# Kernel tuning notes

Hardware: AMD Instinct MI355X
Metric: run time of the kernel (lower is better)

Reference implementation:

```python
import jax, jax.numpy as jnp
import numpy as np

N_NODES = 100000
N_EDGES = 300000
EMB = 256
L = 5
BN_EPS = 1e-5


def setup_inputs() -> dict:
    key = jax.random.key(0)
    ks = jax.random.split(key, 12)
    x = jax.random.randint(ks[0], (N_NODES, 2), 0, 3, dtype=jnp.int64 if jax.config.jax_enable_x64 else jnp.int32)
    edge_index = jax.random.randint(ks[1], (2, N_EDGES), 0, N_NODES)
    edge_attr = jax.random.randint(ks[2], (N_EDGES, 2), 0, 3)
    s = 0.05
    return {
        "x": x,
        "edge_index": edge_index,
        "edge_attr": edge_attr,
        "x_emb1": jax.random.normal(ks[3], (120, EMB), jnp.float32) * s,
        "x_emb2": jax.random.normal(ks[4], (3, EMB), jnp.float32) * s,
        "edge_e1": jax.random.normal(ks[5], (L, 5, EMB), jnp.float32) * s,
        "edge_e2": jax.random.normal(ks[6], (L, 3, EMB), jnp.float32) * s,
        "W1": jax.random.normal(ks[7], (L, EMB, 2 * EMB), jnp.float32) * s,
        "b1": jnp.zeros((L, 2 * EMB), jnp.float32),
        "W2": jax.random.normal(ks[8], (L, 2 * EMB, EMB), jnp.float32) * s,
        "b2": jnp.zeros((L, EMB), jnp.float32),
        "bn_g": jnp.ones((L, EMB), jnp.float32),
        "bn_b": jnp.zeros((L, EMB), jnp.float32),
    }


def reference(x, edge_index, edge_attr, x_emb1, x_emb2, edge_e1, edge_e2, W1, b1, W2, b2, bn_g, bn_b):
    N = x.shape[0]
    loops = jnp.arange(N, dtype=edge_index.dtype)
    src = jnp.concatenate([edge_index[0], loops])  # [E+N]
    dst = jnp.concatenate([edge_index[1], loops])
    # self-loop edge attr = (4, 0)
    ea0 = jnp.concatenate([edge_attr[:, 0], jnp.full((N,), 4, edge_attr.dtype)])
    ea1 = jnp.concatenate([edge_attr[:, 1], jnp.zeros((N,), edge_attr.dtype)])

    # input atom embedding
    h = x_emb1[x[:, 0]] + x_emb2[x[:, 1]]  # [N, EMB]

    for l in range(L):
        ee = edge_e1[l][ea0] + edge_e2[l][ea1]          # [E+N, EMB]
        msg = h[src] + ee                                # gather + edge message
        agg = jax.ops.segment_sum(msg, dst, num_segments=N)  # scatter-add
        # 2-layer MLP update
        hid = jax.nn.relu(agg @ W1[l] + b1[l])
        h2 = hid @ W2[l] + b2[l]
        # BatchNorm1d (training: batch stats, biased variance)
        mean = jnp.mean(h2, axis=0)
        var = jnp.mean(jnp.square(h2 - mean), axis=0)
        h2 = (h2 - mean) * jax.lax.rsqrt(var + BN_EPS) * bn_g[l] + bn_b[l]
        if l < L - 1:
            h2 = jax.nn.relu(h2)
        h = h2  # drop_ratio = 0 -> dropout is identity
    return h
```

## Files before the change

kernel.cpp:

```cpp
#include <hip/hip_runtime.h>

#define NN 100000
#define NNP 100096
#define NE 300000
#define EMB 256
#define NL 5
#define NPART (NNP / 128)
#define BN_EPS 1e-5f

typedef __attribute__((ext_vector_type(8))) _Float16 half8;
typedef __attribute__((ext_vector_type(4))) float f32x4;

__device__ __forceinline__ ushort f2h(float f) {
  _Float16 h = (_Float16)f;
  return *(ushort*)&h;
}
__device__ __forceinline__ float h2f(ushort u) {
  _Float16 h = *(_Float16*)&u;
  return (float)h;
}

__device__ __forceinline__ void gl2lds16(const ushort* g, ushort* l) {
  __builtin_amdgcn_global_load_lds(
      (const __attribute__((address_space(1))) void*)g,
      (__attribute__((address_space(3))) void*)l, 16, 0, 0);
}

__device__ __forceinline__ ushort* lds_at(ushort* base, int row, int bytecol) {
  return (ushort*)((char*)base + row * 128 + (bytecol ^ ((row & 7) << 4)));
}
__device__ __forceinline__ ushort* lds_ct(ushort* base, int row, int bytecol) {
  return (ushort*)((char*)base + row * 256 + (bytecol ^ ((row & 7) << 4)));
}

__global__ __launch_bounds__(256) void k_embed(ushort* __restrict__ hh,
    const int* __restrict__ x, const float* __restrict__ xe1,
    const float* __restrict__ xe2) {
  const int wid = threadIdx.x >> 6, lane = threadIdx.x & 63;
  const int row = blockIdx.x * 4 + wid;
  const int c = lane << 2;
  const int x0 = x[row * 2], x1 = x[row * 2 + 1];
  float4 a = *(const float4*)(xe1 + (size_t)x0 * EMB + c);
  float4 b = *(const float4*)(xe2 + (size_t)x1 * EMB + c);
  ushort4 o;
  o.x = f2h(a.x + b.x); o.y = f2h(a.y + b.y);
  o.z = f2h(a.z + b.z); o.w = f2h(a.w + b.w);
  *(ushort4*)(hh + (size_t)row * EMB + c) = o;
}

__global__ __launch_bounds__(256) void k_hist(int* __restrict__ deg,
    const int* __restrict__ ei) {
  int e = blockIdx.x * 256 + threadIdx.x;
  if (e < NE) atomicAdd(&deg[ei[NE + e]], 1);
}

__global__ __launch_bounds__(1024) void k_scan(const int* __restrict__ deg,
    int* __restrict__ rowptr, int* __restrict__ cursor) {
  __shared__ int wsum[16], woff[17];
  const int t = threadIdx.x;
  const int lane = t & 63, w = t >> 6;
  int base = 0;
  for (int start = 0; start < NN; start += 1024) {
    const int i = start + t;
    const int v0 = (i < NN) ? deg[i] : 0;
    int v = v0;
#pragma unroll
    for (int off = 1; off < 64; off <<= 1) {
      int x = __shfl_up(v, off);
      if (lane >= off) v += x;
    }
    if (lane == 63) wsum[w] = v;
    __syncthreads();
    if (t == 0) {
      int s = 0;
#pragma unroll
      for (int k = 0; k < 16; ++k) { woff[k] = s; s += wsum[k]; }
      woff[16] = s;
    }
    __syncthreads();
    if (i < NN) {
      int excl = base + woff[w] + v - v0;
      rowptr[i] = excl;
      cursor[i] = excl;
    }
    base += woff[16];
    __syncthreads();
  }
  if (t == 0) rowptr[NN] = base;
}

__global__ __launch_bounds__(256) void k_bucket(int* __restrict__ ebuf,
    int* __restrict__ cursor, const int* __restrict__ ei,
    const int* __restrict__ ea) {
  int e = blockIdx.x * 256 + threadIdx.x;
  if (e >= NE) return;
  int src = ei[e], dst = ei[NE + e];
  int c9 = ea[e * 2] * 3 + ea[e * 2 + 1];
  int pos = atomicAdd(&cursor[dst], 1);
  ebuf[pos] = src | (c9 << 20);
}

__global__ __launch_bounds__(256) void k_sortseg(int* __restrict__ ebuf,
    const int* __restrict__ rowptr) {
  int i = blockIdx.x * 256 + threadIdx.x;
  if (i >= NN) return;
  const int beg = rowptr[i], end = rowptr[i + 1];
  for (int a = beg + 1; a < end; ++a) {
    int v = ebuf[a];
    int b = a - 1;
    while (b >= beg && ebuf[b] > v) { ebuf[b + 1] = ebuf[b]; --b; }
    ebuf[b + 1] = v;
  }
}

__global__ __launch_bounds__(256) void k_ecomb(float* __restrict__ ecomb,
    const float* __restrict__ ee1, const float* __restrict__ ee2) {
  const int c = threadIdx.x;
  const int l = blockIdx.x / 10, k = blockIdx.x % 10;
  const float* e1l = ee1 + (size_t)l * 5 * EMB;
  const float* e2l = ee2 + (size_t)l * 3 * EMB;
  float v = (k < 9) ? (e1l[(k / 3) * EMB + c] + e2l[(k % 3) * EMB + c])
                    : (e1l[4 * EMB + c] + e2l[c]);
  ecomb[(size_t)blockIdx.x * EMB + c] = v;
}

__global__ __launch_bounds__(256) void k_wt(const float* __restrict__ src,
    ushort* __restrict__ dst, int R, int C) {
  __shared__ float tile[32][33];
  const int t = threadIdx.x;
  const int tr = t >> 5, tc = t & 31;
  const int r0 = blockIdx.y * 32, c0 = blockIdx.x * 32;
#pragma unroll
  for (int i = 0; i < 4; ++i)
    tile[tr + 8 * i][tc] = src[(size_t)(r0 + tr + 8 * i) * C + c0 + tc];
  __syncthreads();
#pragma unroll
  for (int i = 0; i < 4; ++i)
    dst[(size_t)(c0 + tr + 8 * i) * R + r0 + tc] = f2h(tile[tc][tr + 8 * i]);
}

__global__ __launch_bounds__(256) void k_gather(ushort* __restrict__ aggh,
    const ushort* __restrict__ hh, const int* __restrict__ rowptr,
    const int* __restrict__ ebuf, const float* __restrict__ ecomb) {
  const int wid = threadIdx.x >> 6, lane = threadIdx.x & 63;
  const int i = blockIdx.x * 4 + wid;
  const int c = lane << 2;
  ushort4 hv = *(const ushort4*)(hh + (size_t)i * EMB + c);
  float4 sv = *(const float4*)(ecomb + 9 * EMB + c);
  float sx = h2f(hv.x) + sv.x, sy = h2f(hv.y) + sv.y;
  float sz = h2f(hv.z) + sv.z, sw = h2f(hv.w) + sv.w;
  const int beg = rowptr[i], end = rowptr[i + 1];
  for (int j = beg; j < end; ++j) {
    int p = ebuf[j];
    int src = p & 0xFFFFF, c9 = p >> 20;
    ushort4 a = *(const ushort4*)(hh + (size_t)src * EMB + c);
    float4 b = *(const float4*)(ecomb + (size_t)c9 * EMB + c);
    sx += h2f(a.x) + b.x; sy += h2f(a.y) + b.y;
    sz += h2f(a.z) + b.z; sw += h2f(a.w) + b.w;
  }
  ushort4 o;
  o.x = f2h(sx); o.y = f2h(sy); o.z = f2h(sz); o.w = f2h(sw);
  *(ushort4*)(aggh + (size_t)i * EMB + c) = o;
}


__global__ __launch_bounds__(256) void k_mfma1(
    const ushort* __restrict__ A, const ushort* __restrict__ BT,
    const float* __restrict__ bias, ushort* __restrict__ C) {
  __shared__ ushort smem[16384];
  ushort* As = smem;
  ushort* Bs = smem + 8192;
  const int t = threadIdx.x;
  const int lane = t & 63, w = t >> 6;
  const int wr = w >> 1, wc = w & 1;
  const int m0 = blockIdx.y * 128, n0 = blockIdx.x * 128;
  const int fm = lane & 15, g = lane >> 4;
  const int r_loc = lane >> 3, gchunk = (lane & 7) ^ r_loc;
  f32x4 acc[4][4];
#pragma unroll
  for (int i = 0; i < 4; ++i)
#pragma unroll
    for (int j = 0; j < 4; ++j) acc[i][j] = (f32x4){0.f, 0.f, 0.f, 0.f};

  for (int k0 = 0; k0 < 256; k0 += 64) {
#pragma unroll
    for (int i = 0; i < 4; ++i) {
      const int seg = w * 4 + i;
      const int row = 8 * seg + r_loc;
      gl2lds16(A + (size_t)(m0 + row) * 256 + k0 + gchunk * 8, As + seg * 512);
      gl2lds16(BT + (size_t)(n0 + row) * 256 + k0 + gchunk * 8, Bs + seg * 512);
    }
    __syncthreads();
#pragma unroll
    for (int kk = 0; kk < 2; ++kk) {
      half8 af[4], bf[4];
#pragma unroll
      for (int mi = 0; mi < 4; ++mi)
        af[mi] = *(const half8*)lds_at(As, wr * 64 + mi * 16 + fm,
                                       kk * 64 + g * 16);
#pragma unroll
      for (int ni = 0; ni < 4; ++ni)
        bf[ni] = *(const half8*)lds_at(Bs, wc * 64 + ni * 16 + fm,
                                       kk * 64 + g * 16);
#pragma unroll
      for (int mi = 0; mi < 4; ++mi)
#pragma unroll
        for (int ni = 0; ni < 4; ++ni)
          acc[mi][ni] = __builtin_amdgcn_mfma_f32_16x16x32_f16(
              bf[ni], af[mi], acc[mi][ni], 0, 0, 0);
    }
    __syncthreads();
  }
#pragma unroll
  for (int ni = 0; ni < 4; ++ni) {
    const int col = wc * 64 + ni * 16 + g * 4;
    const float4 b4 = *(const float4*)(bias + n0 + col);
#pragma unroll
    for (int mi = 0; mi < 4; ++mi) {
      const int row = wr * 64 + mi * 16 + fm;
      ushort4 o;
      o.x = f2h(fmaxf(acc[mi][ni].x + b4.x, 0.f));
      o.y = f2h(fmaxf(acc[mi][ni].y + b4.y, 0.f));
      o.z = f2h(fmaxf(acc[mi][ni].z + b4.z, 0.f));
      o.w = f2h(fmaxf(acc[mi][ni].w + b4.w, 0.f));
      *(ushort4*)lds_ct(smem, row, col * 2) = o;
    }
  }
  __syncthreads();
#pragma unroll
  for (int rr = 0; rr < 2; ++rr) {
    const int row = rr * 64 + (t >> 2);
    const int grow = m0 + row;
    if (grow < NN) {
#pragma unroll
      for (int it = 0; it < 4; ++it) {
        const int bc = it * 64 + (t & 3) * 16;
        uint4 v = *(const uint4*)lds_ct(smem, row, bc);
        *(uint4*)((char*)(C + (size_t)grow * 512 + n0) + bc) = v;
      }
    }
  }
}

__global__ __launch_bounds__(256) void k_mfma2(
    const ushort* __restrict__ A, const ushort* __restrict__ BT,
    const float* __restrict__ bias, ushort* __restrict__ hh2,
    float* __restrict__ part_s, float* __restrict__ part_q) {
  __shared__ ushort smem[16384];
  __shared__ float sS[128], sQ[128];
  ushort* As = smem;
  ushort* Bs = smem + 8192;
  const int t = threadIdx.x;
  if (t < 128) { sS[t] = 0.f; sQ[t] = 0.f; }
  const int lane = t & 63, w = t >> 6;
  const int wr = w >> 1, wc = w & 1;
  const int m0 = blockIdx.y * 128, n0 = blockIdx.x * 128;
  const int fm = lane & 15, g = lane >> 4;
  const int r_loc = lane >> 3, gchunk = (lane & 7) ^ r_loc;
  f32x4 acc[4][4];
#pragma unroll
  for (int i = 0; i < 4; ++i)
#pragma unroll
    for (int j = 0; j < 4; ++j) acc[i][j] = (f32x4){0.f, 0.f, 0.f, 0.f};

  for (int k0 = 0; k0 < 512; k0 += 64) {
#pragma unroll
    for (int i = 0; i < 4; ++i) {
      const int seg = w * 4 + i;
      const int row = 8 * seg + r_loc;
      gl2lds16(A + (size_t)(m0 + row) * 512 + k0 + gchunk * 8, As + seg * 512);
      gl2lds16(BT + (size_t)(n0 + row) * 512 + k0 + gchunk * 8, Bs + seg * 512);
    }
    __syncthreads();
#pragma unroll
    for (int kk = 0; kk < 2; ++kk) {
      half8 af[4], bf[4];
#pragma unroll
      for (int mi = 0; mi < 4; ++mi)
        af[mi] = *(const half8*)lds_at(As, wr * 64 + mi * 16 + fm,
                                       kk * 64 + g * 16);
#pragma unroll
      for (int ni = 0; ni < 4; ++ni)
        bf[ni] = *(const half8*)lds_at(Bs, wc * 64 + ni * 16 + fm,
                                       kk * 64 + g * 16);
#pragma unroll
      for (int mi = 0; mi < 4; ++mi)
#pragma unroll
        for (int ni = 0; ni < 4; ++ni)
          acc[mi][ni] = __builtin_amdgcn_mfma_f32_16x16x32_f16(
              bf[ni], af[mi], acc[mi][ni], 0, 0, 0);
    }
    __syncthreads();
  }
#pragma unroll
  for (int ni = 0; ni < 4; ++ni) {
    const int col = wc * 64 + ni * 16 + g * 4;
    const float4 b4 = *(const float4*)(bias + n0 + col);
    float sv[4] = {0.f, 0.f, 0.f, 0.f}, qv[4] = {0.f, 0.f, 0.f, 0.f};
#pragma unroll
    for (int mi = 0; mi < 4; ++mi) {
      const int row = wr * 64 + mi * 16 + fm;
      const float v0 = acc[mi][ni].x + b4.x;
      const float v1 = acc[mi][ni].y + b4.y;
      const float v2 = acc[mi][ni].z + b4.z;
      const float v3 = acc[mi][ni].w + b4.w;
      if (m0 + row < NN) {
        sv[0] += v0; sv[1] += v1; sv[2] += v2; sv[3] += v3;
        qv[0] += v0 * v0; qv[1] += v1 * v1; qv[2] += v2 * v2; qv[3] += v3 * v3;
      }
      ushort4 o;
      o.x = f2h(v0); o.y = f2h(v1); o.z = f2h(v2); o.w = f2h(v3);
      *(ushort4*)lds_ct(smem, row, col * 2) = o;
    }
#pragma unroll
    for (int msk = 1; msk < 16; msk <<= 1) {
#pragma unroll
      for (int j = 0; j < 4; ++j) {
        sv[j] += __shfl_xor(sv[j], msk);
        qv[j] += __shfl_xor(qv[j], msk);
      }
    }
    if (fm == 0) {
#pragma unroll
      for (int j = 0; j < 4; ++j) {
        atomicAdd(&sS[col + j], sv[j]);
        atomicAdd(&sQ[col + j], qv[j]);
      }
    }
  }
  __syncthreads();
#pragma unroll
  for (int rr = 0; rr < 2; ++rr) {
    const int row = rr * 64 + (t >> 2);
    const int grow = m0 + row;
    if (grow < NN) {
#pragma unroll
      for (int it = 0; it < 4; ++it) {
        const int bc = it * 64 + (t & 3) * 16;
        uint4 v = *(const uint4*)lds_ct(smem, row, bc);
        *(uint4*)((char*)(hh2 + (size_t)grow * 256 + n0) + bc) = v;
      }
    }
  }
  if (t < 128) {
    part_s[(size_t)blockIdx.y * 256 + n0 + t] = sS[t];
    part_q[(size_t)blockIdx.y * 256 + n0 + t] = sQ[t];
  }
}

__global__ __launch_bounds__(128) void k_bnfin(float* __restrict__ stats,
    const float* __restrict__ part_s, const float* __restrict__ part_q,
    const float* __restrict__ g, const float* __restrict__ b) {
  const int c = blockIdx.x;
  const int t = threadIdx.x;
  __shared__ float red[4];
  float s = 0.f, q = 0.f;
  for (int r = t; r < NPART; r += 128) {
    s += part_s[(size_t)r * 256 + c];
    q += part_q[(size_t)r * 256 + c];
  }
#pragma unroll
  for (int m = 1; m < 64; m <<= 1) {
    s += __shfl_xor(s, m);
    q += __shfl_xor(q, m);
  }
  if ((t & 63) == 0) { red[(t >> 6) * 2] = s; red[(t >> 6) * 2 + 1] = q; }
  __syncthreads();
  if (t == 0) {
    float st = red[0] + red[2];
    float qt = red[1] + red[3];
    float mean = st * (1.0f / NN);
    float var = qt * (1.0f / NN) - mean * mean;
    float A = g[c] * rsqrtf(var + BN_EPS);
    stats[c] = A;
    stats[256 + c] = b[c] - mean * A;
  }
}

__global__ __launch_bounds__(256) void k_bnapply(
    const ushort* __restrict__ hh2, const float* __restrict__ stats,
    ushort* __restrict__ hh, float* __restrict__ hout, int mode) {
  const int wid = threadIdx.x >> 6, lane = threadIdx.x & 63;
  const int row = blockIdx.x * 4 + wid;
  const int c = lane << 2;
  ushort4 v4 = *(const ushort4*)(hh2 + (size_t)row * EMB + c);
  float4 Av = *(const float4*)(stats + c);
  float4 Bv = *(const float4*)(stats + 256 + c);
  float o0 = fmaf(h2f(v4.x), Av.x, Bv.x);
  float o1 = fmaf(h2f(v4.y), Av.y, Bv.y);
  float o2 = fmaf(h2f(v4.z), Av.z, Bv.z);
  float o3 = fmaf(h2f(v4.w), Av.w, Bv.w);
  if (mode == 0) {
    ushort4 o;
    o.x = f2h(fmaxf(o0, 0.f)); o.y = f2h(fmaxf(o1, 0.f));
    o.z = f2h(fmaxf(o2, 0.f)); o.w = f2h(fmaxf(o3, 0.f));
    *(ushort4*)(hh + (size_t)row * EMB + c) = o;
  } else {
    *(float4*)(hout + (size_t)row * EMB + c) = make_float4(o0, o1, o2, o3);
  }
}

extern "C" void kernel_launch(void* const* d_in, const int* in_sizes, int n_in,
                              void* d_out, int out_size, void* d_ws, size_t ws_size,
                              hipStream_t stream) {
  const int* x    = (const int*)d_in[0];
  const int* ei   = (const int*)d_in[1];
  const int* ea   = (const int*)d_in[2];
  const float* xe1 = (const float*)d_in[3];
  const float* xe2 = (const float*)d_in[4];
  const float* ee1 = (const float*)d_in[5];
  const float* ee2 = (const float*)d_in[6];
  const float* W1  = (const float*)d_in[7];
  const float* b1  = (const float*)d_in[8];
  const float* W2  = (const float*)d_in[9];
  const float* b2  = (const float*)d_in[10];
  const float* bng = (const float*)d_in[11];
  const float* bnb = (const float*)d_in[12];

  char* ws = (char*)d_ws;
  size_t off = 0;
  ushort* aggh = (ushort*)(ws + off); off += (size_t)NNP * 256 * 2;
  ushort* hh2  = (ushort*)(ws + off); off += (size_t)NNP * 256 * 2;
  ushort* hid  = (ushort*)(ws + off); off += (size_t)NNP * 512 * 2;
  ushort* hh   = (ushort*)(ws + off); off += (size_t)NNP * 256 * 2;
  ushort* w1t  = (ushort*)(ws + off); off += (size_t)NL * 512 * 256 * 2;
  ushort* w2t  = (ushort*)(ws + off); off += (size_t)NL * 256 * 512 * 2;
  float* ecomb = (float*)(ws + off); off += (size_t)NL * 10 * EMB * 4;
  float* stats = (float*)(ws + off); off += 512 * 4;
  float* part_s = (float*)(ws + off); off += (size_t)NPART * 256 * 4;
  float* part_q = (float*)(ws + off); off += (size_t)NPART * 256 * 4;
  int* rowptr = (int*)(ws + off); off += (size_t)(NN + 1) * 4;
  int* cursor = (int*)(ws + off); off += (size_t)NN * 4;
  int* ebuf   = (int*)(ws + off); off += (size_t)NE * 4;
  int* deg = ebuf;

  hipMemsetAsync(deg, 0, NN * sizeof(int), stream);
  k_hist<<<(NE + 255) / 256, 256, 0, stream>>>(deg, ei);
  k_scan<<<1, 1024, 0, stream>>>(deg, rowptr, cursor);
  k_bucket<<<(NE + 255) / 256, 256, 0, stream>>>(ebuf, cursor, ei, ea);
  k_sortseg<<<(NN + 255) / 256, 256, 0, stream>>>(ebuf, rowptr);
  k_ecomb<<<NL * 10, 256, 0, stream>>>(ecomb, ee1, ee2);
  for (int l = 0; l < NL; ++l) {
    k_wt<<<dim3(512 / 32, 256 / 32), 256, 0, stream>>>(
        W1 + (size_t)l * 256 * 512, w1t + (size_t)l * 512 * 256, 256, 512);
    k_wt<<<dim3(256 / 32, 512 / 32), 256, 0, stream>>>(
        W2 + (size_t)l * 512 * 256, w2t + (size_t)l * 256 * 512, 512, 256);
  }
  k_embed<<<NN / 4, 256, 0, stream>>>(hh, x, xe1, xe2);

  for (int l = 0; l < NL; ++l) {
    k_gather<<<NN / 4, 256, 0, stream>>>(aggh, hh, rowptr, ebuf,
                                         ecomb + (size_t)l * 10 * EMB);
    k_mfma1<<<dim3(4, NNP / 128), 256, 0, stream>>>(
        aggh, w1t + (size_t)l * 512 * 256, b1 + (size_t)l * 512, hid);
    k_mfma2<<<dim3(2, NNP / 128), 256, 0, stream>>>(
        hid, w2t + (size_t)l * 256 * 512, b2 + (size_t)l * 256, hh2,
        part_s, part_q);
    k_bnfin<<<256, 128, 0, stream>>>(stats, part_s, part_q,
                                     bng + (size_t)l * EMB, bnb + (size_t)l * EMB);
    k_bnapply<<<NN / 4, 256, 0, stream>>>(hh2, stats, hh, (float*)d_out,
                                          l == NL - 1 ? 1 : 0);
  }
}
```

Before: 1.229 ms.

## Fuse BN apply+ReLU into next layer's gather and parallelize degree scan

```diff
diff --git a/kernel.cpp b/kernel.cpp
--- a/kernel.cpp
+++ b/kernel.cpp
@@ -6,6 +6,7 @@
 #define EMB 256
 #define NL 5
 #define NPART (NNP / 128)
+#define NBLK 98
 #define BN_EPS 1e-5f
 
 typedef __attribute__((ext_vector_type(8))) _Float16 half8;
@@ -54,39 +55,77 @@
   if (e < NE) atomicAdd(&deg[ei[NE + e]], 1);
 }
 
-__global__ __launch_bounds__(1024) void k_scan(const int* __restrict__ deg,
-    int* __restrict__ rowptr, int* __restrict__ cursor) {
-  __shared__ int wsum[16], woff[17];
+__global__ __launch_bounds__(256) void k_scan_a(const int* __restrict__ deg,
+    int* __restrict__ bsum) {
+  const int t = threadIdx.x, blk = blockIdx.x;
+  const int base = blk * 1024 + t * 4;
+  int s = 0;
+#pragma unroll
+  for (int j = 0; j < 4; ++j) {
+    int i = base + j;
+    if (i < NN) s += deg[i];
+  }
+  __shared__ int ws[4];
+#pragma unroll
+  for (int m = 1; m < 64; m <<= 1) s += __shfl_xor(s, m);
+  if ((t & 63) == 0) ws[t >> 6] = s;
+  __syncthreads();
+  if (t == 0) bsum[blk] = ws[0] + ws[1] + ws[2] + ws[3];
+}
+
+__global__ __launch_bounds__(128) void k_scan_b(const int* __restrict__ bsum,
+    int* __restrict__ boff, int* __restrict__ rowptr) {
   const int t = threadIdx.x;
   const int lane = t & 63, w = t >> 6;
-  int base = 0;
-  for (int start = 0; start < NN; start += 1024) {
-    const int i = start + t;
-    const int v0 = (i < NN) ? deg[i] : 0;
-    int v = v0;
-#pragma unroll
-    for (int off = 1; off < 64; off <<= 1) {
-      int x = __shfl_up(v, off);
-      if (lane >= off) v += x;
-    }
-    if (lane == 63) wsum[w] = v;
-    __syncthreads();
-    if (t == 0) {
-      int s = 0;
-#pragma unroll
-      for (int k = 0; k < 16; ++k) { woff[k] = s; s += wsum[k]; }
-      woff[16] = s;
-    }
-    __syncthreads();
-    if (i < NN) {
-      int excl = base + woff[w] + v - v0;
-      rowptr[i] = excl;
-      cursor[i] = excl;
-    }
-    base += woff[16];
-    __syncthreads();
-  }
-  if (t == 0) rowptr[NN] = base;
+  __shared__ int wtot[2];
+  int v = (t < NBLK) ? bsum[t] : 0;
+  int inc = v;
+#pragma unroll
+  for (int off = 1; off < 64; off <<= 1) {
+    int x = __shfl_up(inc, off);
+    if (lane >= off) inc += x;
+  }
+  if (lane == 63) wtot[w] = inc;
+  __syncthreads();
+  int add = (w == 1) ? wtot[0] : 0;
+  if (t < NBLK) boff[t] = inc - v + add;
+  if (t == 0) rowptr[NN] = wtot[0] + wtot[1];
+}
+
+__global__ __launch_bounds__(256) void k_scan_c(const int* __restrict__ deg,
+    const int* __restrict__ boff, int* __restrict__ rowptr,
+    int* __restrict__ cursor) {
+  const int t = threadIdx.x, blk = blockIdx.x;
+  const int lane = t & 63, w = t >> 6;
+  const int base = blk * 1024 + t * 4;
+  int v[4];
+  int s = 0;
+#pragma unroll
+  for (int j = 0; j < 4; ++j) {
+    int i = base + j;
+    v[j] = (i < NN) ? deg[i] : 0;
+    s += v[j];
+  }
+  int inc = s;
+#pragma unroll
+  for (int off = 1; off < 64; off <<= 1) {
+    int x = __shfl_up(inc, off);
+    if (lane >= off) inc += x;
+  }
+  __shared__ int wsum[4];
+  if (lane == 63) wsum[w] = inc;
+  __syncthreads();
+  int wadd = 0;
+#pragma unroll
+  for (int k = 0; k < 4; ++k)
+    if (k < w) wadd += wsum[k];
+  int excl = boff[blk] + wadd + inc - s;
+#pragma unroll
+  for (int j = 0; j < 4; ++j) {
+    int i = base + j;
+    if (i < NN) { rowptr[i] = excl; cursor[i] = excl; }
+    excl += v[j];
+  }
 }
 
 __global__ __launch_bounds__(256) void k_bucket(int* __restrict__ ebuf,
@@ -140,23 +179,42 @@
 }
 
 __global__ __launch_bounds__(256) void k_gather(ushort* __restrict__ aggh,
-    const ushort* __restrict__ hh, const int* __restrict__ rowptr,
-    const int* __restrict__ ebuf, const float* __restrict__ ecomb) {
+    const ushort* __restrict__ src_h, const int* __restrict__ rowptr,
+    const int* __restrict__ ebuf, const float* __restrict__ ecomb,
+    const float* __restrict__ stats, int fuse) {
   const int wid = threadIdx.x >> 6, lane = threadIdx.x & 63;
   const int i = blockIdx.x * 4 + wid;
   const int c = lane << 2;
-  ushort4 hv = *(const ushort4*)(hh + (size_t)i * EMB + c);
+  float4 Av = make_float4(1.f, 1.f, 1.f, 1.f);
+  float4 Bv = make_float4(0.f, 0.f, 0.f, 0.f);
+  if (fuse) {
+    Av = *(const float4*)(stats + c);
+    Bv = *(const float4*)(stats + 256 + c);
+  }
+  ushort4 hv = *(const ushort4*)(src_h + (size_t)i * EMB + c);
   float4 sv = *(const float4*)(ecomb + 9 * EMB + c);
-  float sx = h2f(hv.x) + sv.x, sy = h2f(hv.y) + sv.y;
-  float sz = h2f(hv.z) + sv.z, sw = h2f(hv.w) + sv.w;
+  float hx = h2f(hv.x), hy = h2f(hv.y), hz = h2f(hv.z), hw = h2f(hv.w);
+  if (fuse) {
+    hx = fmaxf(fmaf(hx, Av.x, Bv.x), 0.f);
+    hy = fmaxf(fmaf(hy, Av.y, Bv.y), 0.f);
+    hz = fmaxf(fmaf(hz, Av.z, Bv.z), 0.f);
+    hw = fmaxf(fmaf(hw, Av.w, Bv.w), 0.f);
+  }
+  float sx = hx + sv.x, sy = hy + sv.y, sz = hz + sv.z, sw = hw + sv.w;
   const int beg = rowptr[i], end = rowptr[i + 1];
   for (int j = beg; j < end; ++j) {
     int p = ebuf[j];
     int src = p & 0xFFFFF, c9 = p >> 20;
-    ushort4 a = *(const ushort4*)(hh + (size_t)src * EMB + c);
+    ushort4 a = *(const ushort4*)(src_h + (size_t)src * EMB + c);
     float4 b = *(const float4*)(ecomb + (size_t)c9 * EMB + c);
-    sx += h2f(a.x) + b.x; sy += h2f(a.y) + b.y;
-    sz += h2f(a.z) + b.z; sw += h2f(a.w) + b.w;
+    float ax = h2f(a.x), ay = h2f(a.y), az = h2f(a.z), aw = h2f(a.w);
+    if (fuse) {
+      ax = fmaxf(fmaf(ax, Av.x, Bv.x), 0.f);
+      ay = fmaxf(fmaf(ay, Av.y, Bv.y), 0.f);
+      az = fmaxf(fmaf(az, Av.z, Bv.z), 0.f);
+      aw = fmaxf(fmaf(aw, Av.w, Bv.w), 0.f);
+    }
+    sx += ax + b.x; sy += ay + b.y; sz += az + b.z; sw += aw + b.w;
   }
   ushort4 o;
   o.x = f2h(sx); o.y = f2h(sy); o.z = f2h(sz); o.w = f2h(sw);
@@ -379,25 +437,19 @@
 
 __global__ __launch_bounds__(256) void k_bnapply(
     const ushort* __restrict__ hh2, const float* __restrict__ stats,
-    ushort* __restrict__ hh, float* __restrict__ hout, int mode) {
+    float* __restrict__ hout) {
   const int wid = threadIdx.x >> 6, lane = threadIdx.x & 63;
   const int row = blockIdx.x * 4 + wid;
   const int c = lane << 2;
   ushort4 v4 = *(const ushort4*)(hh2 + (size_t)row * EMB + c);
   float4 Av = *(const float4*)(stats + c);
   float4 Bv = *(const float4*)(stats + 256 + c);
-  float o0 = fmaf(h2f(v4.x), Av.x, Bv.x);
-  float o1 = fmaf(h2f(v4.y), Av.y, Bv.y);
-  float o2 = fmaf(h2f(v4.z), Av.z, Bv.z);
-  float o3 = fmaf(h2f(v4.w), Av.w, Bv.w);
-  if (mode == 0) {
-    ushort4 o;
-    o.x = f2h(fmaxf(o0, 0.f)); o.y = f2h(fmaxf(o1, 0.f));
-    o.z = f2h(fmaxf(o2, 0.f)); o.w = f2h(fmaxf(o3, 0.f));
-    *(ushort4*)(hh + (size_t)row * EMB + c) = o;
-  } else {
-    *(float4*)(hout + (size_t)row * EMB + c) = make_float4(o0, o1, o2, o3);
-  }
+  float4 o;
+  o.x = fmaf(h2f(v4.x), Av.x, Bv.x);
+  o.y = fmaf(h2f(v4.y), Av.y, Bv.y);
+  o.z = fmaf(h2f(v4.z), Av.z, Bv.z);
+  o.w = fmaf(h2f(v4.w), Av.w, Bv.w);
+  *(float4*)(hout + (size_t)row * EMB + c) = o;
 }
 
 extern "C" void kernel_launch(void* const* d_in, const int* in_sizes, int n_in,
@@ -431,12 +483,16 @@
   float* part_q = (float*)(ws + off); off += (size_t)NPART * 256 * 4;
   int* rowptr = (int*)(ws + off); off += (size_t)(NN + 1) * 4;
   int* cursor = (int*)(ws + off); off += (size_t)NN * 4;
+  int* bsum = (int*)(ws + off); off += (size_t)(NBLK + 2) * 4;
+  int* boff = (int*)(ws + off); off += (size_t)(NBLK + 2) * 4;
   int* ebuf   = (int*)(ws + off); off += (size_t)NE * 4;
   int* deg = ebuf;
 
   hipMemsetAsync(deg, 0, NN * sizeof(int), stream);
   k_hist<<<(NE + 255) / 256, 256, 0, stream>>>(deg, ei);
-  k_scan<<<1, 1024, 0, stream>>>(deg, rowptr, cursor);
+  k_scan_a<<<NBLK, 256, 0, stream>>>(deg, bsum);
+  k_scan_b<<<1, 128, 0, stream>>>(bsum, boff, rowptr);
+  k_scan_c<<<NBLK, 256, 0, stream>>>(deg, boff, rowptr, cursor);
   k_bucket<<<(NE + 255) / 256, 256, 0, stream>>>(ebuf, cursor, ei, ea);
   k_sortseg<<<(NN + 255) / 256, 256, 0, stream>>>(ebuf, rowptr);
   k_ecomb<<<NL * 10, 256, 0, stream>>>(ecomb, ee1, ee2);
@@ -449,8 +505,9 @@
   k_embed<<<NN / 4, 256, 0, stream>>>(hh, x, xe1, xe2);
 
   for (int l = 0; l < NL; ++l) {
-    k_gather<<<NN / 4, 256, 0, stream>>>(aggh, hh, rowptr, ebuf,
-                                         ecomb + (size_t)l * 10 * EMB);
+    k_gather<<<NN / 4, 256, 0, stream>>>(
+        aggh, l == 0 ? hh : hh2, rowptr, ebuf,
+        ecomb + (size_t)l * 10 * EMB, stats, l == 0 ? 0 : 1);
     k_mfma1<<<dim3(4, NNP / 128), 256, 0, stream>>>(
         aggh, w1t + (size_t)l * 512 * 256, b1 + (size_t)l * 512, hid);
     k_mfma2<<<dim3(2, NNP / 128), 256, 0, stream>>>(
@@ -458,7 +515,6 @@
         part_s, part_q);
     k_bnfin<<<256, 128, 0, stream>>>(stats, part_s, part_q,
                                      bng + (size_t)l * EMB, bnb + (size_t)l * EMB);
-    k_bnapply<<<NN / 4, 256, 0, stream>>>(hh2, stats, hh, (float*)d_out,
-                                          l == NL - 1 ? 1 : 0);
-  }
-}
+  }
+  k_bnapply<<<NN / 4, 256, 0, stream>>>(hh2, stats, (float*)d_out);
+}
```

New measurement: 1.069 ms. 13.1% less time.
